# Kernel tuning notes

Measured on AMD Instinct MI355X. Metric: run time of the kernel, lower is better.

The kernel has to match this reference:

```python
import jax, jax.numpy as jnp
import numpy as np

DIM = 384
HD = 64
SCALE = float(HD ** 0.5)


def _linear_params(key, out_f, in_f):
    kw, kb = jax.random.split(key)
    bound = 1.0 / np.sqrt(in_f)
    W = jax.random.uniform(kw, (out_f, in_f), jnp.float32, -bound, bound)
    b = jax.random.uniform(kb, (out_f,), jnp.float32, -bound, bound)
    return W, b


def setup_inputs() -> dict:
    key = jax.random.key(0)
    ks = jax.random.split(key, 12)
    N = 8192
    situation = jax.random.normal(ks[0], (DIM,), jnp.float32)
    turn_embeddings = jax.random.normal(ks[1], (N, DIM), jnp.float32)
    bilinear_scores = jax.random.normal(ks[2], (N,), jnp.float32)
    Wt, bt = _linear_params(ks[3], HD, DIM + 1)      # turn_proj
    Ws, bs = _linear_params(ks[4], HD, DIM)          # situation_proj
    Wsaq, bsaq = _linear_params(ks[5], HD, HD)
    Wsak, bsak = _linear_params(ks[6], HD, HD)
    Wsav, bsav = _linear_params(ks[7], HD, HD)
    Wcq, bcq = _linear_params(ks[8], HD, HD)
    Wck, bck = _linear_params(ks[9], HD, HD)
    Wcv, bcv = _linear_params(ks[10], HD, HD)
    # score_head is zero-initialized in the module; use small random values so
    # the output is non-trivial for kernel correctness testing.
    Wsc, bsc = _linear_params(ks[11], 1, HD)
    residual_gate = jnp.float32(-5.0)
    return dict(situation=situation, turn_embeddings=turn_embeddings,
                bilinear_scores=bilinear_scores,
                Wt=Wt, bt=bt, Ws=Ws, bs=bs,
                Wsaq=Wsaq, bsaq=bsaq, Wsak=Wsak, bsak=bsak, Wsav=Wsav, bsav=bsav,
                Wcq=Wcq, bcq=bcq, Wck=Wck, bck=bck, Wcv=Wcv, bcv=bcv,
                Wsc=Wsc, bsc=bsc, residual_gate=residual_gate)


def reference(situation, turn_embeddings, bilinear_scores,
              Wt, bt, Ws, bs,
              Wsaq, bsaq, Wsak, bsak, Wsav, bsav,
              Wcq, bcq, Wck, bck, Wcv, bcv,
              Wsc, bsc, residual_gate):
    # [N, dim+1] = [turn_embedding; bilinear_score]
    turn_features = jnp.concatenate([turn_embeddings, bilinear_scores[:, None]], axis=-1)
    turn_hidden = turn_features @ Wt.T + bt                      # [N, HD]
    # self-attention among turns (dropout = identity, eval mode)
    sa_q = turn_hidden @ Wsaq.T + bsaq
    sa_k = turn_hidden @ Wsak.T + bsak
    sa_v = turn_hidden @ Wsav.T + bsav
    sa_weights = jax.nn.softmax((sa_q @ sa_k.T) / SCALE, axis=-1)  # [N, N]
    turn_hidden = turn_hidden + sa_weights @ sa_v
    # sigmoid cross-attention against the single situation vector
    sit_hidden = (situation @ Ws.T + bs)[None, :]                # [1, HD]
    ca_q = turn_hidden @ Wcq.T + bcq                             # [N, HD]
    ca_k = sit_hidden @ Wck.T + bck                              # [1, HD]
    ca_v = sit_hidden @ Wcv.T + bcv                              # [1, HD]
    ca_weights = jax.nn.sigmoid((ca_q @ ca_k.T) / SCALE)         # [N, 1]
    combined = turn_hidden + ca_weights * ca_v                   # [N, HD]
    attention_scores = (combined @ Wsc.T + bsc)[:, 0]            # [N]
    gate = jax.nn.sigmoid(residual_gate)
    return (1.0 - gate) * bilinear_scores + gate * attention_scores
```

## Files before the change

### kernel.cpp

```cpp
#include <hip/hip_runtime.h>
#include <hip/hip_bf16.h>

typedef __attribute__((ext_vector_type(8))) short short8;
typedef __attribute__((ext_vector_type(4))) float f32x4;

__device__ __forceinline__ short f2bf(float x) {
  union { float f; unsigned u; } a; a.f = x;
  unsigned r = (a.u + 0x7FFFu + ((a.u >> 16) & 1u)) >> 16;
  return (short)r;
}
__device__ __forceinline__ float bf2f(short x) {
  union { unsigned u; float f; } a; a.u = ((unsigned)(unsigned short)x) << 16;
  return a.f;
}
__device__ __forceinline__ unsigned cvtpk(float lo, float hi) {
  unsigned r;
  asm("v_cvt_pk_bf16_f32 %0, %1, %2" : "=v"(r) : "v"(lo), "v"(hi));
  return r;
}
__device__ __forceinline__ void gload16(const void* g, void* l) {
  __builtin_amdgcn_global_load_lds((const __attribute__((address_space(1))) unsigned int*)g,
                                   (__attribute__((address_space(3))) unsigned int*)l, 16, 0, 0);
}

__global__ __launch_bounds__(256) void ca_proj3(
    const float* __restrict__ te, const float* __restrict__ bil,
    const float* __restrict__ Wt, const float* __restrict__ bt,
    const float* __restrict__ Wsaq, const float* __restrict__ bq,
    const float* __restrict__ Wsak, const float* __restrict__ bk2,
    const float* __restrict__ Wsav, const float* __restrict__ bv,
    short* __restrict__ hb, short* __restrict__ qb, short* __restrict__ kb,
    short* __restrict__ vt,
    const float* __restrict__ sit, const float* __restrict__ Ws, const float* __restrict__ bs,
    const float* __restrict__ Wck, const float* __restrict__ bck,
    const float* __restrict__ Wcv, const float* __restrict__ bcv,
    const float* __restrict__ Wcq, const float* __restrict__ bcq,
    const float* __restrict__ Wsc, float* __restrict__ u_ws, float* __restrict__ scal,
    int N) {
  __shared__ float Pp[8192];
  __shared__ short Hl[32][72];
  __shared__ short Vt[64][40];
  __shared__ float part[4][64];
  __shared__ float sh[64], ck[64], cv[64];
  const int t = threadIdx.x;
  if ((int)blockIdx.x == (N >> 5)) {
    int j = t & 63, p = t >> 6;
    float a = 0.f;
    for (int d = p * 96; d < p * 96 + 96; ++d) a += Ws[j * 384 + d] * sit[d];
    part[p][j] = a;
    __syncthreads();
    if (t < 64) sh[t] = part[0][t] + part[1][t] + part[2][t] + part[3][t] + bs[t];
    __syncthreads();
    if (t < 64) {
      float kk = bck[t], vv = bcv[t];
      for (int d = 0; d < 64; ++d) { kk += Wck[t * 64 + d] * sh[d]; vv += Wcv[t * 64 + d] * sh[d]; }
      ck[t] = kk; cv[t] = vv;
    }
    __syncthreads();
    if (t < 64) {
      float uu = 0.f;
      for (int jj = 0; jj < 64; ++jj) uu += Wcq[jj * 64 + t] * ck[jj];
      u_ws[t] = uu;
    }
    if (t == 0) {
      float c0 = 0.f, cw = 0.f;
      for (int jj = 0; jj < 64; ++jj) { c0 += bcq[jj] * ck[jj]; cw += cv[jj] * Wsc[jj]; }
      scal[0] = c0; scal[1] = cw;
    }
    return;
  }
  const int lane = t & 63, w = t >> 6;
  const int g = lane >> 4, li = lane & 15;
  const int i0 = blockIdx.x * 32;

  f32x4 acc[2][4];
#pragma unroll
  for (int qs = 0; qs < 2; ++qs)
#pragma unroll
    for (int n = 0; n < 4; ++n) acc[qs][n] = (f32x4){0.f, 0.f, 0.f, 0.f};
  const int kw = w * 96;
#pragma unroll
  for (int ks = 0; ks < 3; ++ks) {
    short8 af[2];
#pragma unroll
    for (int qs = 0; qs < 2; ++qs) {
      const float* ap = te + (size_t)(i0 + qs * 16 + li) * 384 + kw + ks * 32 + g * 8;
      float4 a0 = *(const float4*)ap;
      float4 a1 = *(const float4*)(ap + 4);
      af[qs][0] = f2bf(a0.x); af[qs][1] = f2bf(a0.y); af[qs][2] = f2bf(a0.z); af[qs][3] = f2bf(a0.w);
      af[qs][4] = f2bf(a1.x); af[qs][5] = f2bf(a1.y); af[qs][6] = f2bf(a1.z); af[qs][7] = f2bf(a1.w);
    }
#pragma unroll
    for (int n = 0; n < 4; ++n) {
      short8 bf;
      const float* wp = Wt + (size_t)(n * 16 + li) * 385 + kw + ks * 32 + g * 8;
#pragma unroll
      for (int jj = 0; jj < 8; ++jj) bf[jj] = f2bf(wp[jj]);
      acc[0][n] = __builtin_amdgcn_mfma_f32_16x16x32_bf16(af[0], bf, acc[0][n], 0, 0, 0);
      acc[1][n] = __builtin_amdgcn_mfma_f32_16x16x32_bf16(af[1], bf, acc[1][n], 0, 0, 0);
    }
  }
#pragma unroll
  for (int qs = 0; qs < 2; ++qs)
#pragma unroll
    for (int n = 0; n < 4; ++n)
      *(f32x4*)&Pp[((w * 8 + qs * 4 + n) * 64 + lane) * 4] = acc[qs][n];
  __syncthreads();
#pragma unroll
  for (int ss = 0; ss < 2; ++ss) {
    int s = t + ss * 256;
    int qs2 = s >> 8, n2 = (s >> 6) & 3, lane2 = s & 63;
    int g2 = lane2 >> 4, li2 = lane2 & 15;
    int base = (qs2 * 4 + n2) * 256 + lane2 * 4;
    f32x4 v0 = *(const f32x4*)&Pp[base];
    f32x4 v1 = *(const f32x4*)&Pp[base + 2048];
    f32x4 v2 = *(const f32x4*)&Pp[base + 4096];
    f32x4 v3 = *(const f32x4*)&Pp[base + 6144];
    int col = n2 * 16 + li2;
    float wc = Wt[(size_t)col * 385 + 384], bb = bt[col];
#pragma unroll
    for (int r = 0; r < 4; ++r) {
      int row = qs2 * 16 + g2 * 4 + r;
      float val = v0[r] + v1[r] + v2[r] + v3[r] + bb + bil[i0 + row] * wc;
      Hl[row][col] = f2bf(val);
    }
  }
  __syncthreads();
  {
    int row = t >> 3, seg = t & 7;
    *(uint4*)&hb[(size_t)(i0 + row) * 64 + seg * 8] = *(uint4*)&Hl[row][seg * 8];
  }
  short8 ha[2][2];
#pragma unroll
  for (int qs = 0; qs < 2; ++qs)
#pragma unroll
    for (int ks = 0; ks < 2; ++ks)
      ha[qs][ks] = *(const short8*)&Hl[qs * 16 + li][ks * 32 + g * 8];
  const float* Wm[3] = {Wsaq, Wsak, Wsav};
  f32x4 pacc[3][2];
#pragma unroll
  for (int m = 0; m < 3; ++m)
#pragma unroll
    for (int qs = 0; qs < 2; ++qs) pacc[m][qs] = (f32x4){0.f, 0.f, 0.f, 0.f};
#pragma unroll
  for (int m = 0; m < 3; ++m)
#pragma unroll
    for (int ks = 0; ks < 2; ++ks) {
      const float* wp = Wm[m] + (size_t)(w * 16 + li) * 64 + ks * 32 + g * 8;
      float4 b0 = *(const float4*)wp;
      float4 b1 = *(const float4*)(wp + 4);
      short8 bf;
      bf[0] = f2bf(b0.x); bf[1] = f2bf(b0.y); bf[2] = f2bf(b0.z); bf[3] = f2bf(b0.w);
      bf[4] = f2bf(b1.x); bf[5] = f2bf(b1.y); bf[6] = f2bf(b1.z); bf[7] = f2bf(b1.w);
      pacc[m][0] = __builtin_amdgcn_mfma_f32_16x16x32_bf16(ha[0][ks], bf, pacc[m][0], 0, 0, 0);
      pacc[m][1] = __builtin_amdgcn_mfma_f32_16x16x32_bf16(ha[1][ks], bf, pacc[m][1], 0, 0, 0);
    }
  const int col = w * 16 + li;
  const float QSC = 0.18033688011112042f;
  {
    float bbq = bq[col], bbk = bk2[col], bbv = bv[col];
#pragma unroll
    for (int qs = 0; qs < 2; ++qs)
#pragma unroll
      for (int r = 0; r < 4; ++r) {
        int row = i0 + qs * 16 + g * 4 + r;
        qb[(size_t)row * 64 + col] = f2bf((pacc[0][qs][r] + bbq) * QSC);
        kb[(size_t)row * 64 + col] = f2bf(pacc[1][qs][r] + bbk);
        Vt[col][qs * 16 + g * 4 + r] = f2bf(pacc[2][qs][r] + bbv);
      }
  }
  __syncthreads();
  {
    int c = t >> 2, seg = t & 3;
    *(uint4*)&vt[(size_t)c * N + i0 + seg * 8] = *(uint4*)&Vt[c][seg * 8];
  }
}

__global__ __launch_bounds__(256, 2) void ca_attn6(
    const short* __restrict__ qb, const short* __restrict__ kb, const short* __restrict__ vt,
    unsigned* __restrict__ pOu, float* __restrict__ pL, int N) {
  __shared__ short Kl[2][4096];
  __shared__ short Vl[2][4096];
  __shared__ short Pl[4][32][72];
  const int t = threadIdx.x, lane = t & 63, wid = t >> 6;
  const int g = lane >> 4, li = lane & 15;
  const int bid = blockIdx.x;
  const int sp = (bid >> 1) & 7;
  const int qblk = (bid >> 4) * 2 + (bid & 1);
  const int i0 = qblk * 128 + wid * 32;
  const int k0 = sp * (N >> 3);
  const int ntil = N >> 9;

  const short* ksrc = kb + ((size_t)(wid * 16 + li)) * 64 + g * 8;
  const short* vsrc0 = vt + (size_t)(li + ((2 * wid) & 3) * 16) * N + (wid >> 1) * 32 + g * 8;
  const short* vsrc1 = vt + (size_t)(li + ((2 * wid + 1) & 3) * 16) * N + (wid >> 1) * 32 + g * 8;

#define STAGE_TILE(b, j0)                                                \
  do {                                                                   \
    gload16(ksrc + (size_t)(j0) * 64,       &Kl[b][(2 * wid) * 512]);    \
    gload16(ksrc + (size_t)(j0) * 64 + 32,  &Kl[b][(2 * wid + 1) * 512]);\
    gload16(vsrc0 + (j0),                   &Vl[b][(2 * wid) * 512]);    \
    gload16(vsrc1 + (j0),                   &Vl[b][(2 * wid + 1) * 512]);\
  } while (0)

  short8 qa[2][2];
#pragma unroll
  for (int qs = 0; qs < 2; ++qs)
#pragma unroll
    for (int ks = 0; ks < 2; ++ks)
      qa[qs][ks] = *(const short8*)&qb[(size_t)(i0 + qs * 16 + li) * 64 + g * 8 + ks * 32];

  f32x4 acc[2][4];
  float rs[2] = {0.f, 0.f};
#pragma unroll
  for (int qs = 0; qs < 2; ++qs)
#pragma unroll
    for (int n = 0; n < 4; ++n) acc[qs][n] = (f32x4){0.f, 0.f, 0.f, 0.f};

  STAGE_TILE(0, k0);
  asm volatile("s_waitcnt vmcnt(0)" ::: "memory");

  for (int tt = 0; tt < ntil; ++tt) {
    const int cur = tt & 1;
    __builtin_amdgcn_s_barrier();
    if (tt + 1 < ntil) STAGE_TILE(cur ^ 1, k0 + (tt + 1) * 64);

    f32x4 s4[2][4];
#pragma unroll
    for (int qs = 0; qs < 2; ++qs)
#pragma unroll
      for (int t4 = 0; t4 < 4; ++t4) s4[qs][t4] = (f32x4){0.f, 0.f, 0.f, 0.f};
    __builtin_amdgcn_s_setprio(1);
#pragma unroll
    for (int ks = 0; ks < 2; ++ks)
#pragma unroll
      for (int t4 = 0; t4 < 4; ++t4) {
        short8 kf = *(const short8*)&Kl[cur][(t4 * 2 + ks) * 512 + lane * 8];
        s4[0][t4] = __builtin_amdgcn_mfma_f32_16x16x32_bf16(kf, qa[0][ks], s4[0][t4], 0, 0, 0);
        s4[1][t4] = __builtin_amdgcn_mfma_f32_16x16x32_bf16(kf, qa[1][ks], s4[1][t4], 0, 0, 0);
      }
    __builtin_amdgcn_s_setprio(0);
#pragma unroll
    for (int qs = 0; qs < 2; ++qs) {
#pragma unroll
      for (int t4 = 0; t4 < 4; ++t4) {
        float p0, p1, p2, p3;
        asm("v_exp_f32 %0, %1" : "=v"(p0) : "v"(s4[qs][t4][0]));
        asm("v_exp_f32 %0, %1" : "=v"(p1) : "v"(s4[qs][t4][1]));
        asm("v_exp_f32 %0, %1" : "=v"(p2) : "v"(s4[qs][t4][2]));
        asm("v_exp_f32 %0, %1" : "=v"(p3) : "v"(s4[qs][t4][3]));
        rs[qs] += (p0 + p1) + (p2 + p3);
        uint2 wv;
        wv.x = cvtpk(p0, p1);
        wv.y = cvtpk(p2, p3);
        *(uint2*)&Pl[wid][qs * 16 + li][t4 * 16 + g * 4] = wv;
      }
    }
    asm volatile("s_waitcnt lgkmcnt(0)" ::: "memory");
    short8 pa[2][2];
#pragma unroll
    for (int qs = 0; qs < 2; ++qs)
#pragma unroll
      for (int ks2 = 0; ks2 < 2; ++ks2)
        pa[qs][ks2] = *(const short8*)&Pl[wid][qs * 16 + li][g * 8 + ks2 * 32];
    __builtin_amdgcn_s_setprio(1);
#pragma unroll
    for (int ks2 = 0; ks2 < 2; ++ks2)
#pragma unroll
      for (int dt = 0; dt < 4; ++dt) {
        short8 vf = *(const short8*)&Vl[cur][(ks2 * 4 + dt) * 512 + lane * 8];
        acc[0][dt] = __builtin_amdgcn_mfma_f32_16x16x32_bf16(pa[0][ks2], vf, acc[0][dt], 0, 0, 0);
        acc[1][dt] = __builtin_amdgcn_mfma_f32_16x16x32_bf16(pa[1][ks2], vf, acc[1][dt], 0, 0, 0);
      }
    __builtin_amdgcn_s_setprio(0);
    asm volatile("s_waitcnt vmcnt(0)" ::: "memory");
  }

  const size_t ob = ((size_t)sp * (N >> 5) + (i0 >> 5)) * 2;
#pragma unroll
  for (int qs = 0; qs < 2; ++qs) {
#pragma unroll
    for (int dt = 0; dt < 4; ++dt) {
      uint2 wv;
      wv.x = cvtpk(acc[qs][dt][0], acc[qs][dt][1]);
      wv.y = cvtpk(acc[qs][dt][2], acc[qs][dt][3]);
      *(uint2*)&pOu[((ob + qs) * 4 + dt) * 128 + lane * 2] = wv;
    }
    float r2 = rs[qs] + __shfl_xor(rs[qs], 16, 64);
    r2 += __shfl_xor(r2, 32, 64);
    if (lane < 16) pL[(size_t)sp * N + i0 + qs * 16 + lane] = r2;
  }
#undef STAGE_TILE
}

__global__ __launch_bounds__(256) void ca_merge2(
    const short* __restrict__ hb, const unsigned* __restrict__ pOu, const float* __restrict__ pL,
    const float* __restrict__ u_ws, const float* __restrict__ scal,
    const float* __restrict__ bil, const float* __restrict__ Wsc,
    const float* __restrict__ bsc_p, const float* __restrict__ rgate_p,
    float* __restrict__ out, int N) {
  const int t = threadIdx.x;
  const int qblk = blockIdx.x;
  const int rp = t >> 3, e = t & 7;
  const int dt2 = e >> 1, li0 = (e & 1) * 8;
  const float gate = 1.f / (1.f + __expf(-rgate_p[0]));
  const float bsc = bsc_p[0], sc0 = scal[0], sc1 = scal[1];
#pragma unroll
  for (int pass = 0; pass < 2; ++pass) {
    const int R0 = qblk * 128 + pass * 64 + rp * 2;
    const int b32 = R0 >> 5, qs2 = (R0 >> 4) & 1, g2 = (R0 >> 2) & 3;
    const int rpair = (R0 & 3) >> 1;
    float o0[8], o1[8], L0 = 0.f, L1 = 0.f;
#pragma unroll
    for (int j = 0; j < 8; ++j) { o0[j] = 0.f; o1[j] = 0.f; }
#pragma unroll
    for (int sp2 = 0; sp2 < 8; ++sp2) {
      size_t base = ((((size_t)sp2 * (N >> 5) + b32) * 2 + qs2) * 4 + dt2) * 128
                    + (g2 * 16 + li0) * 2 + rpair;
#pragma unroll
      for (int j = 0; j < 8; ++j) {
        unsigned u = pOu[base + 2 * j];
        o0[j] += bf2f((short)(u & 0xffff));
        o1[j] += bf2f((short)(u >> 16));
      }
      L0 += pL[(size_t)sp2 * N + R0];
      L1 += pL[(size_t)sp2 * N + R0 + 1];
    }
    const float iL0 = 1.f / L0, iL1 = 1.f / L1;
    const int c0 = dt2 * 16 + li0;
    short8 hv0 = *(const short8*)&hb[(size_t)R0 * 64 + c0];
    short8 hv1 = *(const short8*)&hb[(size_t)(R0 + 1) * 64 + c0];
    float s1a = 0.f, s2a = 0.f, s1b = 0.f, s2b = 0.f;
#pragma unroll
    for (int j = 0; j < 8; ++j) {
      float uwsj = u_ws[c0 + j], wscj = Wsc[c0 + j];
      float h0 = bf2f(hv0[j]) + o0[j] * iL0;
      float h1 = bf2f(hv1[j]) + o1[j] * iL1;
      s1a += h0 * uwsj; s2a += h0 * wscj;
      s1b += h1 * uwsj; s2b += h1 * wscj;
    }
#pragma unroll
    for (int mask = 1; mask < 8; mask <<= 1) {
      s1a += __shfl_xor(s1a, mask, 64);
      s2a += __shfl_xor(s2a, mask, 64);
      s1b += __shfl_xor(s1b, mask, 64);
      s2b += __shfl_xor(s2b, mask, 64);
    }
    if (e == 0) {
      float cawa = 1.f / (1.f + __expf(-(s1a + sc0) * 0.125f));
      float cawb = 1.f / (1.f + __expf(-(s1b + sc0) * 0.125f));
      float scoreA = s2a + cawa * sc1 + bsc;
      float scoreB = s2b + cawb * sc1 + bsc;
      out[R0] = (1.f - gate) * bil[R0] + gate * scoreA;
      out[R0 + 1] = (1.f - gate) * bil[R0 + 1] + gate * scoreB;
    }
  }
}

extern "C" void kernel_launch(void* const* d_in, const int* in_sizes, int n_in,
                              void* d_out, int out_size, void* d_ws, size_t ws_size,
                              hipStream_t stream) {
  const float* sit  = (const float*)d_in[0];
  const float* te   = (const float*)d_in[1];
  const float* bil  = (const float*)d_in[2];
  const float* Wt   = (const float*)d_in[3];
  const float* bt   = (const float*)d_in[4];
  const float* Ws   = (const float*)d_in[5];
  const float* bs   = (const float*)d_in[6];
  const float* Wsaq = (const float*)d_in[7];
  const float* bsaq = (const float*)d_in[8];
  const float* Wsak = (const float*)d_in[9];
  const float* bsak = (const float*)d_in[10];
  const float* Wsav = (const float*)d_in[11];
  const float* bsav = (const float*)d_in[12];
  const float* Wcq  = (const float*)d_in[13];
  const float* bcq  = (const float*)d_in[14];
  const float* Wck  = (const float*)d_in[15];
  const float* bck  = (const float*)d_in[16];
  const float* Wcv  = (const float*)d_in[17];
  const float* bcv  = (const float*)d_in[18];
  const float* Wsc  = (const float*)d_in[19];
  const float* bsc  = (const float*)d_in[20];
  const float* rgate= (const float*)d_in[21];
  const int N = in_sizes[2];

  char* w = (char*)d_ws;
  size_t off = 0;
  short* hbuf  = (short*)(w + off); off += (size_t)N * 64 * 2;
  short* qbuf  = (short*)(w + off); off += (size_t)N * 64 * 2;
  short* kbuf  = (short*)(w + off); off += (size_t)N * 64 * 2;
  short* vtbuf = (short*)(w + off); off += (size_t)N * 64 * 2;
  float* u_ws  = (float*)(w + off); off += 64 * 4;
  float* scal  = (float*)(w + off); off += 4 * 4;
  unsigned* pOu= (unsigned*)(w + off); off += (size_t)8 * N * 64 * 2;
  float* pL    = (float*)(w + off); off += (size_t)8 * N * 4;

  ca_proj3<<<N / 32 + 1, 256, 0, stream>>>(te, bil, Wt, bt, Wsaq, bsaq, Wsak, bsak,
                                           Wsav, bsav, hbuf, qbuf, kbuf, vtbuf,
                                           sit, Ws, bs, Wck, bck, Wcv, bcv, Wcq, bcq, Wsc,
                                           u_ws, scal, N);
  ca_attn6<<<N / 16, 256, 0, stream>>>(qbuf, kbuf, vtbuf, pOu, pL, N);
  ca_merge2<<<N / 128, 256, 0, stream>>>(hbuf, pOu, pL, u_ws, scal, bil, Wsc, bsc, rgate,
                                         (float*)d_out, N);
}
```

Baseline: 62.18 us.

## Switch attention Q/K/V/P to FP8 MFMA with pre-swizzled fragment layouts

The projection kernel now quantizes Q, K and V to FP8 and writes them into fragment-ordered global layouts. The attention kernel can then stage K/V tiles with direct global-to-LDS loads and run 16x16x32 fp8 MFMAs instead of bf16 for both QK^T and PV, with P also packed to FP8. Attention blocks shrink to two waves (N/8 blocks of 128 threads) and the merge kernel handles 64 rows per block. The aim is to halve operand bandwidth and LDS traffic and raise MFMA throughput, at the cost of FP8 precision loss in the scores and probabilities, which may break accuracy tolerance.

```diff
diff --git a/kernel.cpp b/kernel.cpp
--- a/kernel.cpp
+++ b/kernel.cpp
@@ -3,6 +3,7 @@
 
 typedef __attribute__((ext_vector_type(8))) short short8;
 typedef __attribute__((ext_vector_type(4))) float f32x4;
+typedef __attribute__((ext_vector_type(2))) long long2t;
 
 __device__ __forceinline__ short f2bf(float x) {
   union { float f; unsigned u; } a; a.f = x;
@@ -18,19 +19,28 @@
   asm("v_cvt_pk_bf16_f32 %0, %1, %2" : "=v"(r) : "v"(lo), "v"(hi));
   return r;
 }
+__device__ __forceinline__ unsigned pk8(float a, float b, float c, float d) {
+  unsigned lo, hi;
+  asm("v_cvt_pk_fp8_f32 %0, %1, %2" : "=v"(lo) : "v"(a), "v"(b));
+  asm("v_cvt_pk_fp8_f32 %0, %1, %2" : "=v"(hi) : "v"(c), "v"(d));
+  return (lo & 0xffffu) | (hi << 16);
+}
+__device__ __forceinline__ long2t as_l2(uint4 v) {
+  union { uint4 u; long2t l; } cc; cc.u = v; return cc.l;
+}
 __device__ __forceinline__ void gload16(const void* g, void* l) {
   __builtin_amdgcn_global_load_lds((const __attribute__((address_space(1))) unsigned int*)g,
                                    (__attribute__((address_space(3))) unsigned int*)l, 16, 0, 0);
 }
 
-__global__ __launch_bounds__(256) void ca_proj3(
+__global__ __launch_bounds__(256) void ca_proj4(
     const float* __restrict__ te, const float* __restrict__ bil,
     const float* __restrict__ Wt, const float* __restrict__ bt,
     const float* __restrict__ Wsaq, const float* __restrict__ bq,
     const float* __restrict__ Wsak, const float* __restrict__ bk2,
     const float* __restrict__ Wsav, const float* __restrict__ bv,
-    short* __restrict__ hb, short* __restrict__ qb, short* __restrict__ kb,
-    short* __restrict__ vt,
+    short* __restrict__ hb, unsigned char* __restrict__ qb8,
+    unsigned char* __restrict__ kb8, unsigned char* __restrict__ vl8,
     const float* __restrict__ sit, const float* __restrict__ Ws, const float* __restrict__ bs,
     const float* __restrict__ Wck, const float* __restrict__ bck,
     const float* __restrict__ Wcv, const float* __restrict__ bcv,
@@ -39,7 +49,9 @@
     int N) {
   __shared__ float Pp[8192];
   __shared__ short Hl[32][72];
-  __shared__ short Vt[64][40];
+  __shared__ unsigned char Q8[32][72];
+  __shared__ unsigned char K8[32][72];
+  __shared__ unsigned char V8s[64][32];
   __shared__ float part[4][64];
   __shared__ float sh[64], ck[64], cv[64];
   const int t = threadIdx.x;
@@ -160,55 +172,62 @@
   {
     float bbq = bq[col], bbk = bk2[col], bbv = bv[col];
 #pragma unroll
-    for (int qs = 0; qs < 2; ++qs)
+    for (int qs = 0; qs < 2; ++qs) {
+      unsigned uq = pk8((pacc[0][qs][0] + bbq) * QSC, (pacc[0][qs][1] + bbq) * QSC,
+                        (pacc[0][qs][2] + bbq) * QSC, (pacc[0][qs][3] + bbq) * QSC);
+      unsigned uk = pk8(pacc[1][qs][0] + bbk, pacc[1][qs][1] + bbk,
+                        pacc[1][qs][2] + bbk, pacc[1][qs][3] + bbk);
+      unsigned uv = pk8(pacc[2][qs][0] + bbv, pacc[2][qs][1] + bbv,
+                        pacc[2][qs][2] + bbv, pacc[2][qs][3] + bbv);
 #pragma unroll
       for (int r = 0; r < 4; ++r) {
-        int row = i0 + qs * 16 + g * 4 + r;
-        qb[(size_t)row * 64 + col] = f2bf((pacc[0][qs][r] + bbq) * QSC);
-        kb[(size_t)row * 64 + col] = f2bf(pacc[1][qs][r] + bbk);
-        Vt[col][qs * 16 + g * 4 + r] = f2bf(pacc[2][qs][r] + bbv);
+        Q8[qs * 16 + g * 4 + r][col] = (unsigned char)(uq >> (8 * r));
+        K8[qs * 16 + g * 4 + r][col] = (unsigned char)(uk >> (8 * r));
       }
+      *(unsigned*)&V8s[col][qs * 16 + g * 4] = uv;
+    }
   }
   __syncthreads();
   {
-    int c = t >> 2, seg = t & 3;
-    *(uint4*)&vt[(size_t)c * N + i0 + seg * 8] = *(uint4*)&Vt[c][seg * 8];
-  }
-}
-
-__global__ __launch_bounds__(256, 2) void ca_attn6(
-    const short* __restrict__ qb, const short* __restrict__ kb, const short* __restrict__ vt,
+    const int h = t & 1, l2 = (t >> 1) & 63, loc = t >> 7;
+    const int srow = (l2 & 15) + 16 * loc;
+    const int scol = h * 32 + (l2 >> 4) * 8;
+    unsigned long vq = *(const unsigned long*)&Q8[srow][scol];
+    *(unsigned long*)(qb8 + ((size_t)((i0 >> 4) + loc) * 1024 + l2 * 16 + h * 8)) = vq;
+    unsigned long vk = *(const unsigned long*)&K8[srow][scol];
+    *(unsigned long*)(kb8 + ((size_t)((i0 >> 6) * 4 + ((i0 >> 4) & 3) + loc) * 1024 + l2 * 16 + h * 8)) = vk;
+    const int dt = t >> 6, l3 = t & 63;
+    unsigned long vv = *(const unsigned long*)&V8s[dt * 16 + (l3 & 15)][(l3 >> 4) * 8];
+    *(unsigned long*)(vl8 + ((size_t)((i0 >> 6) * 4 + dt) * 1024 + l3 * 16 + ((i0 >> 5) & 1) * 8)) = vv;
+  }
+}
+
+__global__ __launch_bounds__(128, 2) void ca_attn7(
+    const uint4* __restrict__ qb8, const unsigned* __restrict__ kb8,
+    const unsigned* __restrict__ vl8,
     unsigned* __restrict__ pOu, float* __restrict__ pL, int N) {
-  __shared__ short Kl[2][4096];
-  __shared__ short Vl[2][4096];
-  __shared__ short Pl[4][32][72];
+  __shared__ unsigned Kl[2][1024];
+  __shared__ unsigned Vl[2][1024];
+  __shared__ unsigned Pl[2][2][256];
   const int t = threadIdx.x, lane = t & 63, wid = t >> 6;
   const int g = lane >> 4, li = lane & 15;
   const int bid = blockIdx.x;
-  const int sp = (bid >> 1) & 7;
-  const int qblk = (bid >> 4) * 2 + (bid & 1);
-  const int i0 = qblk * 128 + wid * 32;
-  const int k0 = sp * (N >> 3);
+  const int sp = bid & 7, qblk = bid >> 3;
+  const int i0 = qblk * 64 + wid * 32;
   const int ntil = N >> 9;
-
-  const short* ksrc = kb + ((size_t)(wid * 16 + li)) * 64 + g * 8;
-  const short* vsrc0 = vt + (size_t)(li + ((2 * wid) & 3) * 16) * N + (wid >> 1) * 32 + g * 8;
-  const short* vsrc1 = vt + (size_t)(li + ((2 * wid + 1) & 3) * 16) * N + (wid >> 1) * 32 + g * 8;
-
-#define STAGE_TILE(b, j0)                                                \
-  do {                                                                   \
-    gload16(ksrc + (size_t)(j0) * 64,       &Kl[b][(2 * wid) * 512]);    \
-    gload16(ksrc + (size_t)(j0) * 64 + 32,  &Kl[b][(2 * wid + 1) * 512]);\
-    gload16(vsrc0 + (j0),                   &Vl[b][(2 * wid) * 512]);    \
-    gload16(vsrc1 + (j0),                   &Vl[b][(2 * wid + 1) * 512]);\
+  const int tile0 = sp * ntil;
+
+#define STG(b, T)                                                                       \
+  do {                                                                                  \
+    gload16(kb8 + (((size_t)(T) * 4 + 2 * wid) << 8) + lane * 4,     &Kl[b][(2 * wid) * 256]);     \
+    gload16(kb8 + (((size_t)(T) * 4 + 2 * wid + 1) << 8) + lane * 4, &Kl[b][(2 * wid + 1) * 256]); \
+    gload16(vl8 + (((size_t)(T) * 4 + 2 * wid) << 8) + lane * 4,     &Vl[b][(2 * wid) * 256]);     \
+    gload16(vl8 + (((size_t)(T) * 4 + 2 * wid + 1) << 8) + lane * 4, &Vl[b][(2 * wid + 1) * 256]); \
   } while (0)
 
-  short8 qa[2][2];
-#pragma unroll
-  for (int qs = 0; qs < 2; ++qs)
-#pragma unroll
-    for (int ks = 0; ks < 2; ++ks)
-      qa[qs][ks] = *(const short8*)&qb[(size_t)(i0 + qs * 16 + li) * 64 + g * 8 + ks * 32];
+  long2t qf[2];
+  qf[0] = as_l2(qb8[(size_t)((i0 >> 4) + 0) * 64 + lane]);
+  qf[1] = as_l2(qb8[(size_t)((i0 >> 4) + 1) * 64 + lane]);
 
   f32x4 acc[2][4];
   float rs[2] = {0.f, 0.f};
@@ -217,13 +236,13 @@
 #pragma unroll
     for (int n = 0; n < 4; ++n) acc[qs][n] = (f32x4){0.f, 0.f, 0.f, 0.f};
 
-  STAGE_TILE(0, k0);
+  STG(0, tile0);
   asm volatile("s_waitcnt vmcnt(0)" ::: "memory");
 
   for (int tt = 0; tt < ntil; ++tt) {
     const int cur = tt & 1;
     __builtin_amdgcn_s_barrier();
-    if (tt + 1 < ntil) STAGE_TILE(cur ^ 1, k0 + (tt + 1) * 64);
+    if (tt + 1 < ntil) STG(cur ^ 1, tile0 + tt + 1);
 
     f32x4 s4[2][4];
 #pragma unroll
@@ -232,13 +251,13 @@
       for (int t4 = 0; t4 < 4; ++t4) s4[qs][t4] = (f32x4){0.f, 0.f, 0.f, 0.f};
     __builtin_amdgcn_s_setprio(1);
 #pragma unroll
-    for (int ks = 0; ks < 2; ++ks)
-#pragma unroll
-      for (int t4 = 0; t4 < 4; ++t4) {
-        short8 kf = *(const short8*)&Kl[cur][(t4 * 2 + ks) * 512 + lane * 8];
-        s4[0][t4] = __builtin_amdgcn_mfma_f32_16x16x32_bf16(kf, qa[0][ks], s4[0][t4], 0, 0, 0);
-        s4[1][t4] = __builtin_amdgcn_mfma_f32_16x16x32_bf16(kf, qa[1][ks], s4[1][t4], 0, 0, 0);
-      }
+    for (int t4 = 0; t4 < 4; ++t4) {
+      long2t kl = as_l2(*(const uint4*)&Kl[cur][t4 * 256 + lane * 4]);
+      s4[0][t4] = __builtin_amdgcn_mfma_f32_16x16x32_fp8_fp8(kl.x, qf[0].x, s4[0][t4], 0, 0, 0);
+      s4[0][t4] = __builtin_amdgcn_mfma_f32_16x16x32_fp8_fp8(kl.y, qf[0].y, s4[0][t4], 0, 0, 0);
+      s4[1][t4] = __builtin_amdgcn_mfma_f32_16x16x32_fp8_fp8(kl.x, qf[1].x, s4[1][t4], 0, 0, 0);
+      s4[1][t4] = __builtin_amdgcn_mfma_f32_16x16x32_fp8_fp8(kl.y, qf[1].y, s4[1][t4], 0, 0, 0);
+    }
     __builtin_amdgcn_s_setprio(0);
 #pragma unroll
     for (int qs = 0; qs < 2; ++qs) {
@@ -250,31 +269,26 @@
         asm("v_exp_f32 %0, %1" : "=v"(p2) : "v"(s4[qs][t4][2]));
         asm("v_exp_f32 %0, %1" : "=v"(p3) : "v"(s4[qs][t4][3]));
         rs[qs] += (p0 + p1) + (p2 + p3);
-        uint2 wv;
-        wv.x = cvtpk(p0, p1);
-        wv.y = cvtpk(p2, p3);
-        *(uint2*)&Pl[wid][qs * 16 + li][t4 * 16 + g * 4] = wv;
+        unsigned u = pk8(p0, p1, p2, p3);
+        Pl[wid][qs][(li + 16 * ((t4 & 1) * 2 + (g >> 1))) * 4 + (t4 >> 1) * 2 + (g & 1)] = u;
       }
     }
     asm volatile("s_waitcnt lgkmcnt(0)" ::: "memory");
-    short8 pa[2][2];
-#pragma unroll
-    for (int qs = 0; qs < 2; ++qs)
-#pragma unroll
-      for (int ks2 = 0; ks2 < 2; ++ks2)
-        pa[qs][ks2] = *(const short8*)&Pl[wid][qs * 16 + li][g * 8 + ks2 * 32];
-    __builtin_amdgcn_s_setprio(1);
-#pragma unroll
-    for (int ks2 = 0; ks2 < 2; ++ks2)
+#pragma unroll
+    for (int qs = 0; qs < 2; ++qs) {
+      long2t pf = as_l2(*(const uint4*)&Pl[wid][qs][lane * 4]);
+      __builtin_amdgcn_s_setprio(1);
 #pragma unroll
       for (int dt = 0; dt < 4; ++dt) {
-        short8 vf = *(const short8*)&Vl[cur][(ks2 * 4 + dt) * 512 + lane * 8];
-        acc[0][dt] = __builtin_amdgcn_mfma_f32_16x16x32_bf16(pa[0][ks2], vf, acc[0][dt], 0, 0, 0);
-        acc[1][dt] = __builtin_amdgcn_mfma_f32_16x16x32_bf16(pa[1][ks2], vf, acc[1][dt], 0, 0, 0);
+        long2t vf = as_l2(*(const uint4*)&Vl[cur][dt * 256 + lane * 4]);
+        acc[qs][dt] = __builtin_amdgcn_mfma_f32_16x16x32_fp8_fp8(pf.x, vf.x, acc[qs][dt], 0, 0, 0);
+        acc[qs][dt] = __builtin_amdgcn_mfma_f32_16x16x32_fp8_fp8(pf.y, vf.y, acc[qs][dt], 0, 0, 0);
       }
-    __builtin_amdgcn_s_setprio(0);
+      __builtin_amdgcn_s_setprio(0);
+    }
     asm volatile("s_waitcnt vmcnt(0)" ::: "memory");
   }
+#undef STG
 
   const size_t ob = ((size_t)sp * (N >> 5) + (i0 >> 5)) * 2;
 #pragma unroll
@@ -290,70 +304,65 @@
     r2 += __shfl_xor(r2, 32, 64);
     if (lane < 16) pL[(size_t)sp * N + i0 + qs * 16 + lane] = r2;
   }
-#undef STAGE_TILE
-}
-
-__global__ __launch_bounds__(256) void ca_merge2(
+}
+
+__global__ __launch_bounds__(256) void ca_merge3(
     const short* __restrict__ hb, const unsigned* __restrict__ pOu, const float* __restrict__ pL,
     const float* __restrict__ u_ws, const float* __restrict__ scal,
     const float* __restrict__ bil, const float* __restrict__ Wsc,
     const float* __restrict__ bsc_p, const float* __restrict__ rgate_p,
     float* __restrict__ out, int N) {
   const int t = threadIdx.x;
-  const int qblk = blockIdx.x;
   const int rp = t >> 3, e = t & 7;
   const int dt2 = e >> 1, li0 = (e & 1) * 8;
   const float gate = 1.f / (1.f + __expf(-rgate_p[0]));
   const float bsc = bsc_p[0], sc0 = scal[0], sc1 = scal[1];
-#pragma unroll
-  for (int pass = 0; pass < 2; ++pass) {
-    const int R0 = qblk * 128 + pass * 64 + rp * 2;
-    const int b32 = R0 >> 5, qs2 = (R0 >> 4) & 1, g2 = (R0 >> 2) & 3;
-    const int rpair = (R0 & 3) >> 1;
-    float o0[8], o1[8], L0 = 0.f, L1 = 0.f;
-#pragma unroll
-    for (int j = 0; j < 8; ++j) { o0[j] = 0.f; o1[j] = 0.f; }
-#pragma unroll
-    for (int sp2 = 0; sp2 < 8; ++sp2) {
-      size_t base = ((((size_t)sp2 * (N >> 5) + b32) * 2 + qs2) * 4 + dt2) * 128
-                    + (g2 * 16 + li0) * 2 + rpair;
-#pragma unroll
-      for (int j = 0; j < 8; ++j) {
-        unsigned u = pOu[base + 2 * j];
-        o0[j] += bf2f((short)(u & 0xffff));
-        o1[j] += bf2f((short)(u >> 16));
-      }
-      L0 += pL[(size_t)sp2 * N + R0];
-      L1 += pL[(size_t)sp2 * N + R0 + 1];
-    }
-    const float iL0 = 1.f / L0, iL1 = 1.f / L1;
-    const int c0 = dt2 * 16 + li0;
-    short8 hv0 = *(const short8*)&hb[(size_t)R0 * 64 + c0];
-    short8 hv1 = *(const short8*)&hb[(size_t)(R0 + 1) * 64 + c0];
-    float s1a = 0.f, s2a = 0.f, s1b = 0.f, s2b = 0.f;
+  const int R0 = blockIdx.x * 64 + rp * 2;
+  const int b32 = R0 >> 5, qs2 = (R0 >> 4) & 1, g2 = (R0 >> 2) & 3;
+  const int rpair = (R0 & 3) >> 1;
+  float o0[8], o1[8], L0 = 0.f, L1 = 0.f;
+#pragma unroll
+  for (int j = 0; j < 8; ++j) { o0[j] = 0.f; o1[j] = 0.f; }
+#pragma unroll
+  for (int sp2 = 0; sp2 < 8; ++sp2) {
+    size_t base = ((((size_t)sp2 * (N >> 5) + b32) * 2 + qs2) * 4 + dt2) * 128
+                  + (g2 * 16 + li0) * 2 + rpair;
 #pragma unroll
     for (int j = 0; j < 8; ++j) {
-      float uwsj = u_ws[c0 + j], wscj = Wsc[c0 + j];
-      float h0 = bf2f(hv0[j]) + o0[j] * iL0;
-      float h1 = bf2f(hv1[j]) + o1[j] * iL1;
-      s1a += h0 * uwsj; s2a += h0 * wscj;
-      s1b += h1 * uwsj; s2b += h1 * wscj;
-    }
-#pragma unroll
-    for (int mask = 1; mask < 8; mask <<= 1) {
-      s1a += __shfl_xor(s1a, mask, 64);
-      s2a += __shfl_xor(s2a, mask, 64);
-      s1b += __shfl_xor(s1b, mask, 64);
-      s2b += __shfl_xor(s2b, mask, 64);
-    }
-    if (e == 0) {
-      float cawa = 1.f / (1.f + __expf(-(s1a + sc0) * 0.125f));
-      float cawb = 1.f / (1.f + __expf(-(s1b + sc0) * 0.125f));
-      float scoreA = s2a + cawa * sc1 + bsc;
-      float scoreB = s2b + cawb * sc1 + bsc;
-      out[R0] = (1.f - gate) * bil[R0] + gate * scoreA;
-      out[R0 + 1] = (1.f - gate) * bil[R0 + 1] + gate * scoreB;
-    }
+      unsigned u = pOu[base + 2 * j];
+      o0[j] += bf2f((short)(u & 0xffff));
+      o1[j] += bf2f((short)(u >> 16));
+    }
+    L0 += pL[(size_t)sp2 * N + R0];
+    L1 += pL[(size_t)sp2 * N + R0 + 1];
+  }
+  const float iL0 = 1.f / L0, iL1 = 1.f / L1;
+  const int c0 = dt2 * 16 + li0;
+  short8 hv0 = *(const short8*)&hb[(size_t)R0 * 64 + c0];
+  short8 hv1 = *(const short8*)&hb[(size_t)(R0 + 1) * 64 + c0];
+  float s1a = 0.f, s2a = 0.f, s1b = 0.f, s2b = 0.f;
+#pragma unroll
+  for (int j = 0; j < 8; ++j) {
+    float uwsj = u_ws[c0 + j], wscj = Wsc[c0 + j];
+    float h0 = bf2f(hv0[j]) + o0[j] * iL0;
+    float h1 = bf2f(hv1[j]) + o1[j] * iL1;
+    s1a += h0 * uwsj; s2a += h0 * wscj;
+    s1b += h1 * uwsj; s2b += h1 * wscj;
+  }
+#pragma unroll
+  for (int mask = 1; mask < 8; mask <<= 1) {
+    s1a += __shfl_xor(s1a, mask, 64);
+    s2a += __shfl_xor(s2a, mask, 64);
+    s1b += __shfl_xor(s1b, mask, 64);
+    s2b += __shfl_xor(s2b, mask, 64);
+  }
+  if (e == 0) {
+    float cawa = 1.f / (1.f + __expf(-(s1a + sc0) * 0.125f));
+    float cawb = 1.f / (1.f + __expf(-(s1b + sc0) * 0.125f));
+    float scoreA = s2a + cawa * sc1 + bsc;
+    float scoreB = s2b + cawb * sc1 + bsc;
+    out[R0] = (1.f - gate) * bil[R0] + gate * scoreA;
+    out[R0 + 1] = (1.f - gate) * bil[R0 + 1] + gate * scoreB;
   }
 }
 
@@ -386,20 +395,21 @@
 
   char* w = (char*)d_ws;
   size_t off = 0;
-  short* hbuf  = (short*)(w + off); off += (size_t)N * 64 * 2;
-  short* qbuf  = (short*)(w + off); off += (size_t)N * 64 * 2;
-  short* kbuf  = (short*)(w + off); off += (size_t)N * 64 * 2;
-  short* vtbuf = (short*)(w + off); off += (size_t)N * 64 * 2;
-  float* u_ws  = (float*)(w + off); off += 64 * 4;
-  float* scal  = (float*)(w + off); off += 4 * 4;
-  unsigned* pOu= (unsigned*)(w + off); off += (size_t)8 * N * 64 * 2;
-  float* pL    = (float*)(w + off); off += (size_t)8 * N * 4;
-
-  ca_proj3<<<N / 32 + 1, 256, 0, stream>>>(te, bil, Wt, bt, Wsaq, bsaq, Wsak, bsak,
-                                           Wsav, bsav, hbuf, qbuf, kbuf, vtbuf,
+  short* hbuf        = (short*)(w + off);         off += (size_t)N * 64 * 2;
+  unsigned char* qb8 = (unsigned char*)(w + off); off += (size_t)N * 64;
+  unsigned char* kb8 = (unsigned char*)(w + off); off += (size_t)N * 64;
+  unsigned char* vl8 = (unsigned char*)(w + off); off += (size_t)N * 64;
+  float* u_ws        = (float*)(w + off);         off += 64 * 4;
+  float* scal        = (float*)(w + off);         off += 4 * 4;
+  unsigned* pOu      = (unsigned*)(w + off);      off += (size_t)8 * N * 64 * 2;
+  float* pL          = (float*)(w + off);         off += (size_t)8 * N * 4;
+
+  ca_proj4<<<N / 32 + 1, 256, 0, stream>>>(te, bil, Wt, bt, Wsaq, bsaq, Wsak, bsak,
+                                           Wsav, bsav, hbuf, qb8, kb8, vl8,
                                            sit, Ws, bs, Wck, bck, Wcv, bcv, Wcq, bcq, Wsc,
                                            u_ws, scal, N);
-  ca_attn6<<<N / 16, 256, 0, stream>>>(qbuf, kbuf, vtbuf, pOu, pL, N);
-  ca_merge2<<<N / 128, 256, 0, stream>>>(hbuf, pOu, pL, u_ws, scal, bil, Wsc, bsc, rgate,
-                                         (float*)d_out, N);
-}
+  ca_attn7<<<N / 8, 128, 0, stream>>>((const uint4*)qb8, (const unsigned*)kb8,
+                                      (const unsigned*)vl8, pOu, pL, N);
+  ca_merge3<<<N / 64, 256, 0, stream>>>(hbuf, pOu, pL, u_ws, scal, bil, Wsc, bsc, rgate,
+                                        (float*)d_out, N);
+}
```

New measurement: 50.61 us. -18.6%, faster.
